# Performance work log

Measured on AMD Instinct MI355X. Metric: run time of the kernel, lower is better.

## Reference

```python
import jax, jax.numpy as jnp
import numpy as np

NUM_REGIONS = 4
REGION_OVERLAP = 0.25
REGIONAL_WEIGHT = 0.6


def setup_inputs() -> dict:
    key = jax.random.key(0)
    features = jax.random.normal(key, (8, 128, 128, 512), dtype=jnp.float32)
    return {"features": features}


def reference(features):
    # features: (B, H, W, D)
    N = NUM_REGIONS
    rw = REGIONAL_WEIGHT
    B, H, W, D = features.shape

    # Global mean over spatial dims (keepdim, broadcasts over H, W)
    global_feat = features.mean(axis=(1, 2), keepdims=True)  # (B,1,1,D)

    # Overlapping region extraction + per-region mean pooling
    region_h, region_w = H // N, W // N
    oh, ow = int(region_h * REGION_OVERLAP), int(region_w * REGION_OVERLAP)
    sh, sw = region_h - oh, region_w - ow
    means = []
    for i in range(N):            # fixed small grid (4x4 = 16 regions)
        for j in range(N):
            h0, w0 = i * sh, j * sw
            h1, w1 = min(h0 + region_h, H), min(w0 + region_w, W)
            means.append(features[:, h0:h1, w0:w1, :].mean(axis=(1, 2)))
    means = jnp.stack(means, axis=1)  # (B, N*N, D), region index r = i*N + j

    # Gaussian weights: exp(-d^2 / (2*0.5^2)) = exp(-2*d^2), d = |coord - i| / N
    h_coords = jnp.linspace(0.0, N - 1, H)  # (H,)
    w_coords = jnp.linspace(0.0, N - 1, W)  # (W,)
    idx = jnp.arange(N, dtype=jnp.float32)
    hw = jnp.exp(-2.0 * ((h_coords[None, :] - idx[:, None]) / N) ** 2)  # (N,H)
    ww = jnp.exp(-2.0 * ((w_coords[None, :] - idx[:, None]) / N) ** 2)  # (N,W)
    Wmat = (hw[:, None, :, None] * ww[None, :, None, :]).reshape(N * N, H, W)

    wsum = Wmat.sum(axis=0)[None, :, :, None]  # (1,H,W,1)
    # Weighted broadcast-aggregate of region means back to pixels
    agg = jnp.einsum('rhw,brd->bhwd', Wmat, means) / (wsum + 1e-8)

    enhanced = (1.0 - rw) * global_feat + rw * agg + features
    return enhanced
```

## Files before the change

kernel.cpp:

```cpp
#include <hip/hip_runtime.h>
#include <math.h>

#define BB 8
#define HH 128
#define WW 128
#define DD 512

__device__ __forceinline__ float4 f4z() { return make_float4(0.f, 0.f, 0.f, 0.f); }
__device__ __forceinline__ float4 f4add(float4 a, float4 b) {
    return make_float4(a.x + b.x, a.y + b.y, a.z + b.z, a.w + b.w);
}
__device__ __forceinline__ float4 f4fma(float s, float4 a, float4 acc) {
    return make_float4(fmaf(s, a.x, acc.x), fmaf(s, a.y, acc.y),
                       fmaf(s, a.z, acc.z), fmaf(s, a.w, acc.w));
}
__device__ __forceinline__ float4 f4scale(float4 a, float s) {
    return make_float4(a.x * s, a.y * s, a.z * s, a.w * s);
}

__global__ __launch_bounds__(128) void k1_rowsums(const float* __restrict__ f,
                                                  float* __restrict__ rowpart,
                                                  float* __restrict__ rowtot) {
    const int bh = blockIdx.x;
    const int d4 = threadIdx.x * 4;
    const float4* p = (const float4*)(f + (size_t)bh * WW * DD + d4);

    float4 tot = f4z(), r0 = f4z(), r1 = f4z(), r2 = f4z(), r3 = f4z();

#define SEG(W0, W1, STMT)                                  \
    _Pragma("unroll 4")                                    \
    for (int w = (W0); w < (W1); ++w) {                    \
        float4 v = p[(size_t)w * (DD / 4)];                \
        tot = f4add(tot, v);                               \
        STMT                                               \
    }
    SEG(0, 24,   r0 = f4add(r0, v);)
    SEG(24, 32,  r0 = f4add(r0, v); r1 = f4add(r1, v);)
    SEG(32, 48,  r1 = f4add(r1, v);)
    SEG(48, 56,  r1 = f4add(r1, v); r2 = f4add(r2, v);)
    SEG(56, 72,  r2 = f4add(r2, v);)
    SEG(72, 80,  r2 = f4add(r2, v); r3 = f4add(r3, v);)
    SEG(80, 104, r3 = f4add(r3, v);)
    SEG(104, 128, )
#undef SEG

    float4* rp = (float4*)(rowpart + ((size_t)bh * 4) * DD + d4);
    rp[0 * (DD / 4)] = r0;
    rp[1 * (DD / 4)] = r1;
    rp[2 * (DD / 4)] = r2;
    rp[3 * (DD / 4)] = r3;
    *(float4*)(rowtot + (size_t)bh * DD + d4) = tot;
}

__global__ __launch_bounds__(128) void k2_reduce(const float* __restrict__ rowpart,
                                                 const float* __restrict__ rowtot,
                                                 float* __restrict__ means,
                                                 float* __restrict__ gmean) {
    const int blk = blockIdx.x;
    const int d4 = threadIdx.x * 4;
    if (blk < BB * 16) {
        const int b = blk >> 4;
        const int r = blk & 15;
        const int i = r >> 2;
        const int j = r & 3;
        const int h0 = i * 24;
        float4 s = f4z();
#pragma unroll 4
        for (int hh = 0; hh < 32; ++hh) {
            const int bh = b * HH + h0 + hh;
            s = f4add(s, *(const float4*)(rowpart + ((size_t)bh * 4 + j) * DD + d4));
        }
        s = f4scale(s, 1.0f / 1024.0f);
        *(float4*)(means + ((size_t)b * 16 + r) * DD + d4) = s;
    } else {
        const int b = blk - BB * 16;
        float4 s = f4z();
#pragma unroll 4
        for (int h = 0; h < HH; ++h) {
            s = f4add(s, *(const float4*)(rowtot + ((size_t)(b * HH + h)) * DD + d4));
        }
        s = f4scale(s, 1.0f / (float)(HH * WW));
        *(float4*)(gmean + (size_t)b * DD + d4) = s;
    }
}

__global__ __launch_bounds__(128) void k3_output(const float* __restrict__ f,
                                                 const float* __restrict__ means,
                                                 const float* __restrict__ gmean,
                                                 float* __restrict__ out) {
    const int bh = blockIdx.x;
    const int b = bh / HH;
    const int h = bh % HH;
    const int tid = threadIdx.x;
    const int d4 = tid * 4;

    __shared__ float4 sww[WW];
    __shared__ float sinv[WW];

    const float hc = (3.0f / 127.0f) * (float)h;
    float hwv[4];
    float Hs = 0.f;
#pragma unroll
    for (int i = 0; i < 4; ++i) {
        const float t = (hc - (float)i) * 0.25f;
        hwv[i] = __expf(-2.0f * t * t);
        Hs += hwv[i];
    }

    {
        const float wc = (3.0f / 127.0f) * (float)tid;
        float wv[4];
        float Ws = 0.f;
#pragma unroll
        for (int j = 0; j < 4; ++j) {
            const float t = (wc - (float)j) * 0.25f;
            wv[j] = __expf(-2.0f * t * t);
            Ws += wv[j];
        }
        sww[tid] = make_float4(wv[0], wv[1], wv[2], wv[3]);
        sinv[tid] = 1.0f / (Hs * Ws + 1e-8f);
    }
    __syncthreads();

    float4 cs0 = f4z(), cs1 = f4z(), cs2 = f4z(), cs3 = f4z();
#pragma unroll
    for (int i = 0; i < 4; ++i) {
        const float hwi = hwv[i];
        const float4* mrow = (const float4*)(means + ((size_t)b * 16 + i * 4) * DD + d4);
        cs0 = f4fma(hwi, mrow[0 * (DD / 4)], cs0);
        cs1 = f4fma(hwi, mrow[1 * (DD / 4)], cs1);
        cs2 = f4fma(hwi, mrow[2 * (DD / 4)], cs2);
        cs3 = f4fma(hwi, mrow[3 * (DD / 4)], cs3);
    }
    const float4 g = *(const float4*)(gmean + (size_t)b * DD + d4);
    const float4 gterm = f4scale(g, 0.4f);

    const float4* fp = (const float4*)(f + (size_t)bh * WW * DD + d4);
    float4* op = (float4*)(out + (size_t)bh * WW * DD + d4);

#pragma unroll 4
    for (int w = 0; w < WW; ++w) {
        const float4 v = fp[(size_t)w * (DD / 4)];
        const float4 wwv = sww[w];
        const float inv = sinv[w] * 0.6f;
        float4 o;
        o.x = v.x + gterm.x + (cs0.x * wwv.x + cs1.x * wwv.y + cs2.x * wwv.z + cs3.x * wwv.w) * inv;
        o.y = v.y + gterm.y + (cs0.y * wwv.x + cs1.y * wwv.y + cs2.y * wwv.z + cs3.y * wwv.w) * inv;
        o.z = v.z + gterm.z + (cs0.z * wwv.x + cs1.z * wwv.y + cs2.z * wwv.z + cs3.z * wwv.w) * inv;
        o.w = v.w + gterm.w + (cs0.w * wwv.x + cs1.w * wwv.y + cs2.w * wwv.z + cs3.w * wwv.w) * inv;
        op[(size_t)w * (DD / 4)] = o;
    }
}

extern "C" void kernel_launch(void* const* d_in, const int* in_sizes, int n_in,
                              void* d_out, int out_size, void* d_ws, size_t ws_size,
                              hipStream_t stream) {
    const float* f = (const float*)d_in[0];
    float* out = (float*)d_out;

    float* ws = (float*)d_ws;
    float* rowpart = ws;
    float* rowtot = rowpart + (size_t)BB * HH * 4 * DD;
    float* means = rowtot + (size_t)BB * HH * DD;
    float* gmean = means + (size_t)BB * 16 * DD;

    k1_rowsums<<<BB * HH, 128, 0, stream>>>(f, rowpart, rowtot);
    k2_reduce<<<BB * 16 + BB, 128, 0, stream>>>(rowpart, rowtot, means, gmean);
    k3_output<<<BB * HH, 128, 0, stream>>>(f, means, gmean, out);
}
```

Before: 506.8 us.

## Split W-axis across four thread groups per row block with LDS reduction

```diff
diff --git a/kernel.cpp b/kernel.cpp
--- a/kernel.cpp
+++ b/kernel.cpp
@@ -18,38 +18,61 @@
     return make_float4(a.x * s, a.y * s, a.z * s, a.w * s);
 }
 
-__global__ __launch_bounds__(128) void k1_rowsums(const float* __restrict__ f,
+__global__ __launch_bounds__(512) void k1_rowsums(const float* __restrict__ f,
                                                   float* __restrict__ rowpart,
                                                   float* __restrict__ rowtot) {
     const int bh = blockIdx.x;
-    const int d4 = threadIdx.x * 4;
-    const float4* p = (const float4*)(f + (size_t)bh * WW * DD + d4);
+    const int tid = threadIdx.x;
+    const int dt = tid & 127;
+    const int g = tid >> 7;
+    const int d4 = dt * 4;
+
+    const float4* p = (const float4*)(f + (size_t)bh * WW * DD) + (size_t)g * (DD / 4) + dt;
 
     float4 tot = f4z(), r0 = f4z(), r1 = f4z(), r2 = f4z(), r3 = f4z();
 
-#define SEG(W0, W1, STMT)                                  \
-    _Pragma("unroll 4")                                    \
-    for (int w = (W0); w < (W1); ++w) {                    \
-        float4 v = p[(size_t)w * (DD / 4)];                \
+#define SEG(I0, I1, STMT)                                  \
+    _Pragma("unroll")                                      \
+    for (int it = (I0); it < (I1); ++it) {                 \
+        float4 v = p[(size_t)it * 4 * (DD / 4)];           \
         tot = f4add(tot, v);                               \
         STMT                                               \
     }
-    SEG(0, 24,   r0 = f4add(r0, v);)
-    SEG(24, 32,  r0 = f4add(r0, v); r1 = f4add(r1, v);)
-    SEG(32, 48,  r1 = f4add(r1, v);)
-    SEG(48, 56,  r1 = f4add(r1, v); r2 = f4add(r2, v);)
-    SEG(56, 72,  r2 = f4add(r2, v);)
-    SEG(72, 80,  r2 = f4add(r2, v); r3 = f4add(r3, v);)
-    SEG(80, 104, r3 = f4add(r3, v);)
-    SEG(104, 128, )
+    SEG(0, 6,   r0 = f4add(r0, v);)
+    SEG(6, 8,   r0 = f4add(r0, v); r1 = f4add(r1, v);)
+    SEG(8, 12,  r1 = f4add(r1, v);)
+    SEG(12, 14, r1 = f4add(r1, v); r2 = f4add(r2, v);)
+    SEG(14, 18, r2 = f4add(r2, v);)
+    SEG(18, 20, r2 = f4add(r2, v); r3 = f4add(r3, v);)
+    SEG(20, 26, r3 = f4add(r3, v);)
+    SEG(26, 32, )
 #undef SEG
 
-    float4* rp = (float4*)(rowpart + ((size_t)bh * 4) * DD + d4);
-    rp[0 * (DD / 4)] = r0;
-    rp[1 * (DD / 4)] = r1;
-    rp[2 * (DD / 4)] = r2;
-    rp[3 * (DD / 4)] = r3;
-    *(float4*)(rowtot + (size_t)bh * DD + d4) = tot;
+    __shared__ float4 lds[3][5][128];
+    if (g > 0) {
+        lds[g - 1][0][dt] = r0;
+        lds[g - 1][1][dt] = r1;
+        lds[g - 1][2][dt] = r2;
+        lds[g - 1][3][dt] = r3;
+        lds[g - 1][4][dt] = tot;
+    }
+    __syncthreads();
+    if (g == 0) {
+#pragma unroll
+        for (int gg = 0; gg < 3; ++gg) {
+            r0 = f4add(r0, lds[gg][0][dt]);
+            r1 = f4add(r1, lds[gg][1][dt]);
+            r2 = f4add(r2, lds[gg][2][dt]);
+            r3 = f4add(r3, lds[gg][3][dt]);
+            tot = f4add(tot, lds[gg][4][dt]);
+        }
+        float4* rp = (float4*)(rowpart + ((size_t)bh * 4) * DD + d4);
+        rp[0 * (DD / 4)] = r0;
+        rp[1 * (DD / 4)] = r1;
+        rp[2 * (DD / 4)] = r2;
+        rp[3 * (DD / 4)] = r3;
+        *(float4*)(rowtot + (size_t)bh * DD + d4) = tot;
+    }
 }
 
 __global__ __launch_bounds__(128) void k2_reduce(const float* __restrict__ rowpart,
@@ -65,7 +88,7 @@
         const int j = r & 3;
         const int h0 = i * 24;
         float4 s = f4z();
-#pragma unroll 4
+#pragma unroll 8
         for (int hh = 0; hh < 32; ++hh) {
             const int bh = b * HH + h0 + hh;
             s = f4add(s, *(const float4*)(rowpart + ((size_t)bh * 4 + j) * DD + d4));
@@ -75,16 +98,16 @@
     } else {
         const int b = blk - BB * 16;
         float4 s = f4z();
-#pragma unroll 4
+#pragma unroll 8
         for (int h = 0; h < HH; ++h) {
-            s = f4add(s, *(const float4*)(rowtot + ((size_t)(b * HH + h)) * DD + d4));
+            s = f4add(s, *(const float4*)(rowtot + (size_t)(b * HH + h) * DD + d4));
         }
         s = f4scale(s, 1.0f / (float)(HH * WW));
         *(float4*)(gmean + (size_t)b * DD + d4) = s;
     }
 }
 
-__global__ __launch_bounds__(128) void k3_output(const float* __restrict__ f,
+__global__ __launch_bounds__(512) void k3_output(const float* __restrict__ f,
                                                  const float* __restrict__ means,
                                                  const float* __restrict__ gmean,
                                                  float* __restrict__ out) {
@@ -92,7 +115,9 @@
     const int b = bh / HH;
     const int h = bh % HH;
     const int tid = threadIdx.x;
-    const int d4 = tid * 4;
+    const int dt = tid & 127;
+    const int g = tid >> 7;
+    const int d4 = dt * 4;
 
     __shared__ float4 sww[WW];
     __shared__ float sinv[WW];
@@ -107,7 +132,7 @@
         Hs += hwv[i];
     }
 
-    {
+    if (tid < WW) {
         const float wc = (3.0f / 127.0f) * (float)tid;
         float wv[4];
         float Ws = 0.f;
@@ -118,7 +143,7 @@
             Ws += wv[j];
         }
         sww[tid] = make_float4(wv[0], wv[1], wv[2], wv[3]);
-        sinv[tid] = 1.0f / (Hs * Ws + 1e-8f);
+        sinv[tid] = 0.6f / (Hs * Ws + 1e-8f);
     }
     __syncthreads();
 
@@ -132,23 +157,24 @@
         cs2 = f4fma(hwi, mrow[2 * (DD / 4)], cs2);
         cs3 = f4fma(hwi, mrow[3 * (DD / 4)], cs3);
     }
-    const float4 g = *(const float4*)(gmean + (size_t)b * DD + d4);
-    const float4 gterm = f4scale(g, 0.4f);
+    const float4 gv = *(const float4*)(gmean + (size_t)b * DD + d4);
+    const float4 gterm = f4scale(gv, 0.4f);
 
-    const float4* fp = (const float4*)(f + (size_t)bh * WW * DD + d4);
-    float4* op = (float4*)(out + (size_t)bh * WW * DD + d4);
+    const float4* fp = (const float4*)(f + (size_t)bh * WW * DD) + (size_t)g * (DD / 4) + dt;
+    float4* op = (float4*)(out + (size_t)bh * WW * DD) + (size_t)g * (DD / 4) + dt;
 
-#pragma unroll 4
-    for (int w = 0; w < WW; ++w) {
-        const float4 v = fp[(size_t)w * (DD / 4)];
+#pragma unroll 8
+    for (int it = 0; it < 32; ++it) {
+        const int w = it * 4 + g;
+        const float4 v = fp[(size_t)it * 4 * (DD / 4)];
         const float4 wwv = sww[w];
-        const float inv = sinv[w] * 0.6f;
+        const float inv = sinv[w];
         float4 o;
         o.x = v.x + gterm.x + (cs0.x * wwv.x + cs1.x * wwv.y + cs2.x * wwv.z + cs3.x * wwv.w) * inv;
         o.y = v.y + gterm.y + (cs0.y * wwv.x + cs1.y * wwv.y + cs2.y * wwv.z + cs3.y * wwv.w) * inv;
         o.z = v.z + gterm.z + (cs0.z * wwv.x + cs1.z * wwv.y + cs2.z * wwv.z + cs3.z * wwv.w) * inv;
         o.w = v.w + gterm.w + (cs0.w * wwv.x + cs1.w * wwv.y + cs2.w * wwv.z + cs3.w * wwv.w) * inv;
-        op[(size_t)w * (DD / 4)] = o;
+        op[(size_t)it * 4 * (DD / 4)] = o;
     }
 }
 
@@ -164,7 +190,7 @@
     float* means = rowtot + (size_t)BB * HH * DD;
     float* gmean = means + (size_t)BB * 16 * DD;
 
-    k1_rowsums<<<BB * HH, 128, 0, stream>>>(f, rowpart, rowtot);
+    k1_rowsums<<<BB * HH, 512, 0, stream>>>(f, rowpart, rowtot);
     k2_reduce<<<BB * 16 + BB, 128, 0, stream>>>(rowpart, rowtot, means, gmean);
-    k3_output<<<BB * HH, 128, 0, stream>>>(f, means, gmean, out);
+    k3_output<<<BB * HH, 512, 0, stream>>>(f, means, gmean, out);
 }
```

New measurement: 496.0 us. -2.1%, faster.
